# Performance work log

Hardware: AMD Instinct MI355X
Metric: run time of the kernel (lower is better)

The kernel has to match this reference:

```python
import jax, jax.numpy as jnp
import numpy as np
from jax import lax

BATCH, SEQ, IN_F, H_SIZE, OUT_F = 65536, 64, 16, 10, 5

def setup_inputs() -> dict:
    key = jax.random.key(0)
    k1, k2, k3, k4, k5 = jax.random.split(key, 5)
    x = jax.random.uniform(k1, (BATCH, SEQ, IN_F), dtype=jnp.float32)
    W1 = jax.random.normal(k2, (IN_F, H_SIZE), dtype=jnp.float32) * (1.0 / np.sqrt(IN_F))
    b1 = jax.random.normal(k3, (H_SIZE,), dtype=jnp.float32) * 0.02
    W2 = jax.random.normal(k4, (H_SIZE, OUT_F), dtype=jnp.float32) * (1.0 / np.sqrt(H_SIZE))
    b2 = jax.random.normal(k5, (OUT_F,), dtype=jnp.float32) * 0.02
    return {"x": x, "W1": W1, "b1": b1, "W2": W2, "b2": b2}

def reference(x, W1, b1, W2, b2):
    # h_{t} = tanh(h_{t-1} + x_t @ W1 + b1); y = sigmoid(h_T @ W2 + b2)
    b = x.shape[0]
    h0 = jnp.zeros((b, W1.shape[1]), dtype=x.dtype)
    # precompute all input projections in one big GEMM: [B,S,H]
    a = jnp.einsum('bsi,ih->bsh', x, W1) + b1
    def step(h, a_t):
        return jnp.tanh(h + a_t), None
    h, _ = lax.scan(step, h0, jnp.swapaxes(a, 0, 1))  # scan over seq
    return jax.nn.sigmoid(h @ W2 + b2)
```

## Files before the change

kernel.cpp:

```cpp
#include <hip/hip_runtime.h>

#define BATCH 65536
#define SEQ   64
#define INF   16
#define HS    10
#define OUTF  5

#define PIN(v) asm volatile("" : "+v"(v))

__global__ __launch_bounds__(256, 4) void rnn_fused(
    const float* __restrict__ x,  const float* __restrict__ W1,
    const float* __restrict__ b1, const float* __restrict__ W2,
    const float* __restrict__ b2, float* __restrict__ out)
{
    const int g   = blockIdx.x * 256 + threadIdx.x;
    const int row = g >> 2;
    const int j   = g & 3;

    float w1l[4 * HS];
#pragma unroll
    for (int il = 0; il < 4; ++il)
#pragma unroll
        for (int h = 0; h < HS; ++h)
            w1l[il * HS + h] = W1[(4 * j + il) * HS + h];
#pragma unroll
    for (int k = 0; k < 4 * HS; ++k) { PIN(w1l[k]); }

    float bq[HS];
#pragma unroll
    for (int h = 0; h < HS; ++h) { bq[h] = 0.25f * b1[h]; }
#pragma unroll
    for (int h = 0; h < HS; ++h) { PIN(bq[h]); }

    float hreg[HS];
#pragma unroll
    for (int h = 0; h < HS; ++h) hreg[h] = 0.0f;

    const float4* __restrict__ xr =
        reinterpret_cast<const float4*>(x) + (size_t)row * (SEQ * 4) + j;

    float4 buf[4];
#pragma unroll
    for (int r = 0; r < 4; ++r) buf[r] = xr[r * 4];

#pragma unroll 4
    for (int s = 0; s < SEQ; ++s) {
        const int slot = s & 3;
        const float4 xv = buf[slot];
        const int pf = (s + 4 < SEQ) ? (s + 4) : (SEQ - 1);
        buf[slot] = xr[pf * 4];

        float a[HS];
#pragma unroll
        for (int h = 0; h < HS; ++h) a[h] = bq[h];
#pragma unroll
        for (int h = 0; h < HS; ++h) {
            a[h] = fmaf(xv.x, w1l[0 * HS + h], a[h]);
            a[h] = fmaf(xv.y, w1l[1 * HS + h], a[h]);
            a[h] = fmaf(xv.z, w1l[2 * HS + h], a[h]);
            a[h] = fmaf(xv.w, w1l[3 * HS + h], a[h]);
        }
#pragma unroll
        for (int h = 0; h < HS; ++h) a[h] += __shfl_xor(a[h], 1);
#pragma unroll
        for (int h = 0; h < HS; ++h) a[h] += __shfl_xor(a[h], 2);

#pragma unroll
        for (int h = 0; h < HS; ++h) {
            float t = hreg[h] + a[h];
            float e = __expf(2.0f * t);
            hreg[h] = fmaf(-2.0f, __builtin_amdgcn_rcpf(e + 1.0f), 1.0f);
        }
    }

    float y[OUTF];
#pragma unroll
    for (int o = 0; o < OUTF; ++o) y[o] = b2[o];
#pragma unroll
    for (int h = 0; h < HS; ++h)
#pragma unroll
        for (int o = 0; o < OUTF; ++o)
            y[o] = fmaf(hreg[h], W2[h * OUTF + o], y[o]);
#pragma unroll
    for (int o = 0; o < OUTF; ++o)
        y[o] = __builtin_amdgcn_rcpf(1.0f + __expf(-y[o]));

    float* op = out + (size_t)row * OUTF;
    op[j] = y[j];
    if (j == 0) op[4] = y[4];
}

extern "C" void kernel_launch(void* const* d_in, const int* in_sizes, int n_in,
                              void* d_out, int out_size, void* d_ws, size_t ws_size,
                              hipStream_t stream) {
    const float* x  = (const float*)d_in[0];
    const float* W1 = (const float*)d_in[1];
    const float* b1 = (const float*)d_in[2];
    const float* W2 = (const float*)d_in[3];
    const float* b2 = (const float*)d_in[4];
    float* out = (float*)d_out;

    rnn_fused<<<(BATCH * 4) / 256, 256, 0, stream>>>(x, W1, b1, W2, b2, out);
}
```

Measured before the change: 396.1 us.

## Partition hidden units across lanes and shuffle inputs instead of partial sums

Result: faster. 380.9 us (-3.8%).

```diff
diff --git a/kernel.cpp b/kernel.cpp
--- a/kernel.cpp
+++ b/kernel.cpp
@@ -4,9 +4,15 @@
 #define SEQ   64
 #define INF   16
 #define HS    10
+#define UPL   3
 #define OUTF  5
 
 #define PIN(v) asm volatile("" : "+v"(v))
+
+__device__ __forceinline__ float4 shfl_xor4(float4 v, int m) {
+    return make_float4(__shfl_xor(v.x, m), __shfl_xor(v.y, m),
+                       __shfl_xor(v.z, m), __shfl_xor(v.w, m));
+}
 
 __global__ __launch_bounds__(256, 4) void rnn_fused(
     const float* __restrict__ x,  const float* __restrict__ W1,
@@ -17,24 +23,36 @@
     const int row = g >> 2;
     const int j   = g & 3;
 
-    float w1l[4 * HS];
+    float wl[4][4][UPL];
+    float bl[UPL];
 #pragma unroll
-    for (int il = 0; il < 4; ++il)
+    for (int u = 0; u < UPL; ++u) {
+        const int hu = UPL * j + u;
+        const int hc = (hu < HS) ? hu : 0;
+        const bool ok = (hu < HS);
+        bl[u] = ok ? b1[hc] : 0.0f;
 #pragma unroll
-        for (int h = 0; h < HS; ++h)
-            w1l[il * HS + h] = W1[(4 * j + il) * HS + h];
+        for (int m = 0; m < 4; ++m) {
+            const int lm = j ^ m;
 #pragma unroll
-    for (int k = 0; k < 4 * HS; ++k) { PIN(w1l[k]); }
+            for (int k = 0; k < 4; ++k) {
+                const int col = 4 * lm + k;
+                wl[m][k][u] = ok ? W1[col * HS + hc] : 0.0f;
+            }
+        }
+    }
+#pragma unroll
+    for (int m = 0; m < 4; ++m)
+#pragma unroll
+        for (int k = 0; k < 4; ++k)
+#pragma unroll
+            for (int u = 0; u < UPL; ++u) { PIN(wl[m][k][u]); }
+#pragma unroll
+    for (int u = 0; u < UPL; ++u) { PIN(bl[u]); }
 
-    float bq[HS];
+    float h[UPL];
 #pragma unroll
-    for (int h = 0; h < HS; ++h) { bq[h] = 0.25f * b1[h]; }
-#pragma unroll
-    for (int h = 0; h < HS; ++h) { PIN(bq[h]); }
-
-    float hreg[HS];
-#pragma unroll
-    for (int h = 0; h < HS; ++h) hreg[h] = 0.0f;
+    for (int u = 0; u < UPL; ++u) h[u] = 0.0f;
 
     const float4* __restrict__ xr =
         reinterpret_cast<const float4*>(x) + (size_t)row * (SEQ * 4) + j;
@@ -46,44 +64,58 @@
 #pragma unroll 4
     for (int s = 0; s < SEQ; ++s) {
         const int slot = s & 3;
-        const float4 xv = buf[slot];
+        const float4 g0 = buf[slot];
         const int pf = (s + 4 < SEQ) ? (s + 4) : (SEQ - 1);
         buf[slot] = xr[pf * 4];
 
-        float a[HS];
-#pragma unroll
-        for (int h = 0; h < HS; ++h) a[h] = bq[h];
-#pragma unroll
-        for (int h = 0; h < HS; ++h) {
-            a[h] = fmaf(xv.x, w1l[0 * HS + h], a[h]);
-            a[h] = fmaf(xv.y, w1l[1 * HS + h], a[h]);
-            a[h] = fmaf(xv.z, w1l[2 * HS + h], a[h]);
-            a[h] = fmaf(xv.w, w1l[3 * HS + h], a[h]);
-        }
-#pragma unroll
-        for (int h = 0; h < HS; ++h) a[h] += __shfl_xor(a[h], 1);
-#pragma unroll
-        for (int h = 0; h < HS; ++h) a[h] += __shfl_xor(a[h], 2);
+        const float4 g1 = shfl_xor4(g0, 1);
+        const float4 g2 = shfl_xor4(g0, 2);
+        const float4 g3 = shfl_xor4(g0, 3);
 
 #pragma unroll
-        for (int h = 0; h < HS; ++h) {
-            float t = hreg[h] + a[h];
-            float e = __expf(2.0f * t);
-            hreg[h] = fmaf(-2.0f, __builtin_amdgcn_rcpf(e + 1.0f), 1.0f);
+        for (int u = 0; u < UPL; ++u) {
+            float p0 = fmaf(g0.x, wl[0][0][u], bl[u]);
+            p0 = fmaf(g0.y, wl[0][1][u], p0);
+            p0 = fmaf(g0.z, wl[0][2][u], p0);
+            p0 = fmaf(g0.w, wl[0][3][u], p0);
+            float p1 = g1.x * wl[1][0][u];
+            p1 = fmaf(g1.y, wl[1][1][u], p1);
+            p1 = fmaf(g1.z, wl[1][2][u], p1);
+            p1 = fmaf(g1.w, wl[1][3][u], p1);
+            float p2 = g2.x * wl[2][0][u];
+            p2 = fmaf(g2.y, wl[2][1][u], p2);
+            p2 = fmaf(g2.z, wl[2][2][u], p2);
+            p2 = fmaf(g2.w, wl[2][3][u], p2);
+            float p3 = g3.x * wl[3][0][u];
+            p3 = fmaf(g3.y, wl[3][1][u], p3);
+            p3 = fmaf(g3.z, wl[3][2][u], p3);
+            p3 = fmaf(g3.w, wl[3][3][u], p3);
+            const float a = (p0 + p1) + (p2 + p3);
+
+            const float t = h[u] + a;
+            const float e = __expf(t + t);
+            h[u] = fmaf(-2.0f, __builtin_amdgcn_rcpf(e + 1.0f), 1.0f);
         }
     }
 
     float y[OUTF];
 #pragma unroll
-    for (int o = 0; o < OUTF; ++o) y[o] = b2[o];
+    for (int o = 0; o < OUTF; ++o) y[o] = 0.0f;
 #pragma unroll
-    for (int h = 0; h < HS; ++h)
+    for (int u = 0; u < UPL; ++u) {
+        const int hu = UPL * j + u;
+        const float* w2r = W2 + (size_t)((hu < HS) ? hu : 0) * OUTF;
 #pragma unroll
         for (int o = 0; o < OUTF; ++o)
-            y[o] = fmaf(hreg[h], W2[h * OUTF + o], y[o]);
+            y[o] = fmaf(h[u], w2r[o], y[o]);
+    }
+#pragma unroll
+    for (int o = 0; o < OUTF; ++o) y[o] += __shfl_xor(y[o], 1);
+#pragma unroll
+    for (int o = 0; o < OUTF; ++o) y[o] += __shfl_xor(y[o], 2);
 #pragma unroll
     for (int o = 0; o < OUTF; ++o)
-        y[o] = __builtin_amdgcn_rcpf(1.0f + __expf(-y[o]));
+        y[o] = __builtin_amdgcn_rcpf(1.0f + __expf(-(y[o] + b2[o])));
 
     float* op = out + (size_t)row * OUTF;
     op[j] = y[j];
```
